# Kernel tuning notes

Measured on AMD Instinct MI355X. Metric: run time of the kernel, lower is better.

## Reference

```python
import jax, jax.numpy as jnp
import numpy as np

C = 256
C8 = C // 8
B, D, H, W = 2, 16, 64, 64


def setup_inputs() -> dict:
    key = jax.random.key(0)
    ks = jax.random.split(key, 8)
    s = 0.05
    return {
        "x1": jax.random.normal(ks[0], (B, C, D, H, W), dtype=jnp.float32),
        "x2": jax.random.normal(ks[1], (B, C, D, H, W), dtype=jnp.float32),
        "Wq": jax.random.normal(ks[2], (C8, C), dtype=jnp.float32) * s,
        "bq": jax.random.normal(ks[3], (C8,), dtype=jnp.float32) * s,
        "Wk": jax.random.normal(ks[4], (C8, C), dtype=jnp.float32) * s,
        "bk": jax.random.normal(ks[5], (C8,), dtype=jnp.float32) * s,
        "Wv": jax.random.normal(ks[6], (C, C), dtype=jnp.float32) * s,
        "bv": jax.random.normal(ks[7], (C,), dtype=jnp.float32) * s,
    }


def _conv1x1(x, Wt, b):
    # 1x1x1 Conv3d == channel-mixing linear: x [B,Cin,D,H,W], Wt [Cout,Cin]
    return jnp.einsum('bcdhw,oc->bodhw', x, Wt) + b[None, :, None, None, None]


def reference(x1, x2, Wq, bq, Wk, bk, Wv, bv):
    q = _conv1x1(x1, Wq, bq)   # [B,C8,D,H,W]
    k = _conv1x1(x2, Wk, bk)   # [B,C8,D,H,W]
    v = _conv1x1(x2, Wv, bv)   # [B,C, D,H,W]
    # Non-softmax bilinear attention over the W axis, batched over (b,d,h)
    attn = jnp.einsum('bcdhx,bcdhy->bdhxy', q, k)        # [B,D,H,W,W]
    out = jnp.einsum('bdhxy,bcdhy->bcdhx', attn, v)      # [B,C,D,H,W]
    return out
```

## Files before the change

kernel.cpp:

```cpp
#include <hip/hip_runtime.h>

#define NB   2
#define ND   16
#define NH   64
#define DHW  65536
#define HW   4096
#define CDHW 16777216

#define XT_LD 72
#define XL_LD 66
#define QK_LD 40
#define A_LD  72
#define VB_LD 72

#define OFF_XTH 0
#define OFF_XTL 9216
#define OFF_R2  18432
#define OFF_KH  18432
#define OFF_KL  23552
#define OFF_AH  0
#define OFF_AL  9216
#define OFF_QH  36864
#define OFF_QL  41984
#define SMEM_BYTES 47104

typedef __attribute__((ext_vector_type(4))) float f32x4;
typedef __attribute__((ext_vector_type(8))) short bf16x8;
typedef unsigned short ushort_t;

#define MFMA16(a, b, c) __builtin_amdgcn_mfma_f32_16x16x32_bf16((a), (b), (c), 0, 0, 0)

#define WS_WQH 0
#define WS_WQL 8192
#define WS_WKH 16384
#define WS_WKL 24576
#define WS_WVH 32768
#define WS_WVL 98304
#define WS_NEED_BYTES 327680

__device__ __forceinline__ void split_val(float f, short& h, short& l) {
  unsigned int u = __builtin_bit_cast(unsigned int, f);
  h = (short)(unsigned short)(u >> 16);
  float fh = __builtin_bit_cast(float, u & 0xffff0000u);
  float r = f - fh;
  l = (short)(unsigned short)(__builtin_bit_cast(unsigned int, r) >> 16);
}

__device__ __forceinline__ void load_split8(const float* __restrict__ p, bf16x8& h8, bf16x8& l8) {
  float4 a = *(const float4*)p;
  float4 b = *(const float4*)(p + 4);
  float f[8] = {a.x, a.y, a.z, a.w, b.x, b.y, b.z, b.w};
#pragma unroll
  for (int j = 0; j < 8; ++j) {
    short hh, ll;
    split_val(f[j], hh, ll);
    h8[j] = hh; l8[j] = ll;
  }
}

__global__ void prep_w(const float* __restrict__ Wq, const float* __restrict__ Wk,
                       const float* __restrict__ Wv, ushort_t* __restrict__ ws) {
  int idx = blockIdx.x * 256 + threadIdx.x;
  const float* src; int off; ushort_t *H, *L;
  if (idx < 8192)       { src = Wq; off = idx;         H = ws + WS_WQH; L = ws + WS_WQL; }
  else if (idx < 16384) { src = Wk; off = idx - 8192;  H = ws + WS_WKH; L = ws + WS_WKL; }
  else if (idx < 81920) { src = Wv; off = idx - 16384; H = ws + WS_WVH; L = ws + WS_WVL; }
  else return;
  short h, l;
  split_val(src[off], h, l);
  H[off] = (ushort_t)h;
  L[off] = (ushort_t)l;
}

template<bool PW>
__global__ __launch_bounds__(256, 3) void xattn(
    const float* __restrict__ x1, const float* __restrict__ x2,
    const float* __restrict__ Wq, const float* __restrict__ bq,
    const float* __restrict__ Wk, const float* __restrict__ bk,
    const float* __restrict__ Wv, const float* __restrict__ bv,
    const ushort_t* __restrict__ wsp, float* __restrict__ out)
{
  __shared__ char smem[SMEM_BYTES];
  ushort_t* Xth  = (ushort_t*)(smem + OFF_XTH);
  ushort_t* Xtl  = (ushort_t*)(smem + OFF_XTL);
  float*    Xlin = (float*)(smem + OFF_R2);
  ushort_t* Kh   = (ushort_t*)(smem + OFF_KH);
  ushort_t* Kl   = (ushort_t*)(smem + OFF_KL);
  ushort_t* Vb   = (ushort_t*)(smem + OFF_R2);
  ushort_t* Ah   = (ushort_t*)(smem + OFF_AH);
  ushort_t* Al   = (ushort_t*)(smem + OFF_AL);
  ushort_t* Qh   = (ushort_t*)(smem + OFF_QH);
  ushort_t* Ql   = (ushort_t*)(smem + OFF_QL);

  const int tid  = threadIdx.x;
  const int lane = tid & 63;
  const int wv   = tid >> 6;
  const int l15  = lane & 15;
  const int g    = lane >> 4;

  const int grp = blockIdx.x;
  const int b   = grp >> 10;
  const int rem = grp & 1023;
  const int d   = rem >> 6;
  const int h   = rem & 63;
  const size_t base = (size_t)b * CDHW + (size_t)d * HW + (size_t)h * 64;

  const ushort_t* WqH = wsp + WS_WQH;
  const ushort_t* WqL = wsp + WS_WQL;
  const ushort_t* WkH = wsp + WS_WKH;
  const ushort_t* WkL = wsp + WS_WKL;
  const ushort_t* WvH = wsp + WS_WVH;
  const ushort_t* WvL = wsp + WS_WVL;

  auto passA = [&](const float* __restrict__ src) {
#pragma unroll
    for (int i = 0; i < 4; ++i) {
      int ch = 16 * wv + (lane >> 4) + 4 * i;
      int c4 = (lane & 15) << 2;
      float4 v = *(const float4*)(src + (size_t)ch * DHW + c4);
      *(float4*)&Xlin[ch * XL_LD + c4] = v;
    }
  };
  auto passB = [&]() {
#pragma unroll
    for (int bb = 0; bb < 2; ++bb) {
      int c0 = 16 * wv + 8 * bb;
      bf16x8 h8, l8;
#pragma unroll
      for (int j = 0; j < 8; ++j) {
        float f = Xlin[(c0 + j) * XL_LD + lane];
        short hh, ll;
        split_val(f, hh, ll);
        h8[j] = hh; l8[j] = ll;
      }
      *(bf16x8*)&Xth[lane * XT_LD + c0] = h8;
      *(bf16x8*)&Xtl[lane * XT_LD + c0] = l8;
    }
  };

  {
    f32x4 qacc[2];
#pragma unroll
    for (int mt = 0; mt < 2; ++mt) {
      int r0 = mt * 16 + 4 * g;
      qacc[mt] = (f32x4){bq[r0], bq[r0 + 1], bq[r0 + 2], bq[r0 + 3]};
    }
    for (int t = 0; t < 4; ++t) {
      passA(x1 + base + (size_t)t * 64 * DHW);
      __syncthreads();
      passB();
      __syncthreads();
#pragma unroll
      for (int ks = 0; ks < 2; ++ks) {
        const int ko = ks * 32 + 8 * g;
        const int kg = t * 64 + ko;
        bf16x8 bh = *(const bf16x8*)&Xth[(16 * wv + l15) * XT_LD + ko];
        bf16x8 bl = *(const bf16x8*)&Xtl[(16 * wv + l15) * XT_LD + ko];
#pragma unroll
        for (int mt = 0; mt < 2; ++mt) {
          bf16x8 wh, wl;
          if constexpr (PW) {
            wh = *(const bf16x8*)&WqH[(size_t)(mt * 16 + l15) * 256 + kg];
            wl = *(const bf16x8*)&WqL[(size_t)(mt * 16 + l15) * 256 + kg];
          } else {
            load_split8(Wq + (size_t)(mt * 16 + l15) * 256 + kg, wh, wl);
          }
          qacc[mt] = MFMA16(wh, bh, qacc[mt]);
          qacc[mt] = MFMA16(wh, bl, qacc[mt]);
          qacc[mt] = MFMA16(wl, bh, qacc[mt]);
        }
      }
      __syncthreads();
    }
    const int x = 16 * wv + l15;
#pragma unroll
    for (int mt = 0; mt < 2; ++mt)
#pragma unroll
      for (int r = 0; r < 4; ++r) {
        short hh, ll;
        split_val(qacc[mt][r], hh, ll);
        Qh[x * QK_LD + mt * 16 + 4 * g + r] = (ushort_t)hh;
        Ql[x * QK_LD + mt * 16 + 4 * g + r] = (ushort_t)ll;
      }
  }

  f32x4 vacc[4][4];
  {
    f32x4 kacc[2];
#pragma unroll
    for (int mt = 0; mt < 2; ++mt) {
      int r0 = mt * 16 + 4 * g;
      kacc[mt] = (f32x4){bk[r0], bk[r0 + 1], bk[r0 + 2], bk[r0 + 3]};
    }
#pragma unroll
    for (int mt = 0; mt < 4; ++mt) {
      int r0 = 64 * wv + mt * 16 + 4 * g;
      f32x4 bb = (f32x4){bv[r0], bv[r0 + 1], bv[r0 + 2], bv[r0 + 3]};
#pragma unroll
      for (int nt = 0; nt < 4; ++nt) vacc[mt][nt] = bb;
    }
    for (int t = 0; t < 4; ++t) {
      passA(x2 + base + (size_t)t * 64 * DHW);
      __syncthreads();
      passB();
      __syncthreads();
#pragma unroll
      for (int ks = 0; ks < 2; ++ks) {
        const int ko = ks * 32 + 8 * g;
        const int kg = t * 64 + ko;
        bf16x8 xh[4], xl[4];
#pragma unroll
        for (int nt = 0; nt < 4; ++nt) {
          xh[nt] = *(const bf16x8*)&Xth[(nt * 16 + l15) * XT_LD + ko];
          xl[nt] = *(const bf16x8*)&Xtl[(nt * 16 + l15) * XT_LD + ko];
        }
        {
          bf16x8 bh = *(const bf16x8*)&Xth[(16 * wv + l15) * XT_LD + ko];
          bf16x8 bl = *(const bf16x8*)&Xtl[(16 * wv + l15) * XT_LD + ko];
#pragma unroll
          for (int mt = 0; mt < 2; ++mt) {
            bf16x8 wh, wl;
            if constexpr (PW) {
              wh = *(const bf16x8*)&WkH[(size_t)(mt * 16 + l15) * 256 + kg];
              wl = *(const bf16x8*)&WkL[(size_t)(mt * 16 + l15) * 256 + kg];
            } else {
              load_split8(Wk + (size_t)(mt * 16 + l15) * 256 + kg, wh, wl);
            }
            kacc[mt] = MFMA16(wh, bh, kacc[mt]);
            kacc[mt] = MFMA16(wh, bl, kacc[mt]);
            kacc[mt] = MFMA16(wl, bh, kacc[mt]);
          }
        }
#pragma unroll
        for (int mt = 0; mt < 4; ++mt) {
          bf16x8 wh, wl;
          if constexpr (PW) {
            wh = *(const bf16x8*)&WvH[(size_t)(64 * wv + mt * 16 + l15) * 256 + kg];
            wl = *(const bf16x8*)&WvL[(size_t)(64 * wv + mt * 16 + l15) * 256 + kg];
          } else {
            load_split8(Wv + (size_t)(64 * wv + mt * 16 + l15) * 256 + kg, wh, wl);
          }
#pragma unroll
          for (int nt = 0; nt < 4; ++nt) {
            vacc[mt][nt] = MFMA16(wh, xh[nt], vacc[mt][nt]);
            vacc[mt][nt] = MFMA16(wh, xl[nt], vacc[mt][nt]);
            vacc[mt][nt] = MFMA16(wl, xh[nt], vacc[mt][nt]);
          }
        }
      }
      __syncthreads();
    }
    const int y = 16 * wv + l15;
#pragma unroll
    for (int mt = 0; mt < 2; ++mt)
#pragma unroll
      for (int r = 0; r < 4; ++r) {
        short hh, ll;
        split_val(kacc[mt][r], hh, ll);
        Kh[y * QK_LD + mt * 16 + 4 * g + r] = (ushort_t)hh;
        Kl[y * QK_LD + mt * 16 + 4 * g + r] = (ushort_t)ll;
      }
  }
  __syncthreads();

  {
    const int y = 16 * wv + l15;
    bf16x8 kh = *(const bf16x8*)&Kh[y * QK_LD + 8 * g];
    bf16x8 kl = *(const bf16x8*)&Kl[y * QK_LD + 8 * g];
    f32x4 acc[4];
#pragma unroll
    for (int mt = 0; mt < 4; ++mt) acc[mt] = (f32x4){0.f, 0.f, 0.f, 0.f};
#pragma unroll
    for (int mt = 0; mt < 4; ++mt) {
      bf16x8 qh = *(const bf16x8*)&Qh[(mt * 16 + l15) * QK_LD + 8 * g];
      bf16x8 ql = *(const bf16x8*)&Ql[(mt * 16 + l15) * QK_LD + 8 * g];
      acc[mt] = MFMA16(qh, kh, acc[mt]);
      acc[mt] = MFMA16(qh, kl, acc[mt]);
      acc[mt] = MFMA16(ql, kh, acc[mt]);
    }
#pragma unroll
    for (int mt = 0; mt < 4; ++mt)
#pragma unroll
      for (int r = 0; r < 4; ++r) {
        short hh, ll;
        split_val(acc[mt][r], hh, ll);
        Ah[(mt * 16 + 4 * g + r) * A_LD + y] = (ushort_t)hh;
        Al[(mt * 16 + 4 * g + r) * A_LD + y] = (ushort_t)ll;
      }
  }
  __syncthreads();

  {
    ushort_t* Vh = Vb + wv * 2304;
    ushort_t* Vl = Vh + 1152;
    const int cb = 64 * wv;
#pragma unroll
    for (int mt = 0; mt < 4; ++mt) {
#pragma unroll
      for (int nt = 0; nt < 4; ++nt)
#pragma unroll
        for (int r = 0; r < 4; ++r) {
          short hh, ll;
          split_val(vacc[mt][nt][r], hh, ll);
          Vh[(4 * g + r) * VB_LD + nt * 16 + l15] = (ushort_t)hh;
          Vl[(4 * g + r) * VB_LD + nt * 16 + l15] = (ushort_t)ll;
        }
      f32x4 oacc[4];
#pragma unroll
      for (int nt = 0; nt < 4; ++nt) oacc[nt] = (f32x4){0.f, 0.f, 0.f, 0.f};
#pragma unroll
      for (int ys = 0; ys < 2; ++ys) {
        const int yo = ys * 32 + 8 * g;
        bf16x8 vh8 = *(const bf16x8*)&Vh[l15 * VB_LD + yo];
        bf16x8 vl8 = *(const bf16x8*)&Vl[l15 * VB_LD + yo];
#pragma unroll
        for (int nt = 0; nt < 4; ++nt) {
          bf16x8 ah8 = *(const bf16x8*)&Ah[(nt * 16 + l15) * A_LD + yo];
          bf16x8 al8 = *(const bf16x8*)&Al[(nt * 16 + l15) * A_LD + yo];
          oacc[nt] = MFMA16(vh8, ah8, oacc[nt]);
          oacc[nt] = MFMA16(vh8, al8, oacc[nt]);
          oacc[nt] = MFMA16(vl8, ah8, oacc[nt]);
        }
      }
#pragma unroll
      for (int nt = 0; nt < 4; ++nt)
#pragma unroll
        for (int r = 0; r < 4; ++r)
          out[base + (size_t)(cb + mt * 16 + 4 * g + r) * DHW + nt * 16 + l15] = oacc[nt][r];
    }
  }
}

extern "C" void kernel_launch(void* const* d_in, const int* in_sizes, int n_in,
                              void* d_out, int out_size, void* d_ws, size_t ws_size,
                              hipStream_t stream)
{
  const float* x1 = (const float*)d_in[0];
  const float* x2 = (const float*)d_in[1];
  const float* Wq = (const float*)d_in[2];
  const float* bq = (const float*)d_in[3];
  const float* Wk = (const float*)d_in[4];
  const float* bk = (const float*)d_in[5];
  const float* Wv = (const float*)d_in[6];
  const float* bv = (const float*)d_in[7];
  float* out = (float*)d_out;

  const bool pw = (ws_size >= (size_t)WS_NEED_BYTES) && (d_ws != nullptr);
  if (pw) {
    ushort_t* ws = (ushort_t*)d_ws;
    hipLaunchKernelGGL(prep_w, dim3(320), dim3(256), 0, stream, Wq, Wk, Wv, ws);
    hipLaunchKernelGGL(xattn<true>, dim3(NB * ND * NH), dim3(256), 0, stream,
                       x1, x2, Wq, bq, Wk, bk, Wv, bv, ws, out);
  } else {
    hipLaunchKernelGGL(xattn<false>, dim3(NB * ND * NH), dim3(256), 0, stream,
                       x1, x2, Wq, bq, Wk, bk, Wv, bv, (const ushort_t*)nullptr, out);
  }
}
```

Baseline: 206.5 us.

## Prefetch input chunks into registers and use XOR-swizzled LDS transpose

Replaces the two-pass staging (global to an fp32 LDS buffer, then transpose and split into bf16 hi/lo tiles) with direct per-lane register loads that are converted in registers and written once into an XOR-swizzled LDS layout. The next chunk's global loads are issued right after the LDS write, so they overlap the MFMA work of the current chunk, and the trailing barrier per iteration is removed. This cuts LDS traffic and one barrier per chunk, and hides global latency. In exchange it costs 16 extra registers per thread for the prefetch buffer, which may put pressure on the 3-blocks-per-CU occupancy target.

```diff
diff --git a/kernel.cpp b/kernel.cpp
--- a/kernel.cpp
+++ b/kernel.cpp
@@ -7,19 +7,17 @@
 #define HW   4096
 #define CDHW 16777216
 
-#define XT_LD 72
-#define XL_LD 66
 #define QK_LD 40
 #define A_LD  72
 #define VB_LD 72
 
 #define OFF_XTH 0
-#define OFF_XTL 9216
+#define OFF_XTL 8192
+#define OFF_AH  0
+#define OFF_AL  9216
 #define OFF_R2  18432
 #define OFF_KH  18432
 #define OFF_KL  23552
-#define OFF_AH  0
-#define OFF_AL  9216
 #define OFF_QH  36864
 #define OFF_QL  41984
 #define SMEM_BYTES 47104
@@ -81,16 +79,15 @@
     const ushort_t* __restrict__ wsp, float* __restrict__ out)
 {
   __shared__ char smem[SMEM_BYTES];
-  ushort_t* Xth  = (ushort_t*)(smem + OFF_XTH);
-  ushort_t* Xtl  = (ushort_t*)(smem + OFF_XTL);
-  float*    Xlin = (float*)(smem + OFF_R2);
-  ushort_t* Kh   = (ushort_t*)(smem + OFF_KH);
-  ushort_t* Kl   = (ushort_t*)(smem + OFF_KL);
-  ushort_t* Vb   = (ushort_t*)(smem + OFF_R2);
-  ushort_t* Ah   = (ushort_t*)(smem + OFF_AH);
-  ushort_t* Al   = (ushort_t*)(smem + OFF_AL);
-  ushort_t* Qh   = (ushort_t*)(smem + OFF_QH);
-  ushort_t* Ql   = (ushort_t*)(smem + OFF_QL);
+  ushort_t* Xth = (ushort_t*)(smem + OFF_XTH);
+  ushort_t* Xtl = (ushort_t*)(smem + OFF_XTL);
+  ushort_t* Kh  = (ushort_t*)(smem + OFF_KH);
+  ushort_t* Kl  = (ushort_t*)(smem + OFF_KL);
+  ushort_t* Vb  = (ushort_t*)(smem + OFF_R2);
+  ushort_t* Ah  = (ushort_t*)(smem + OFF_AH);
+  ushort_t* Al  = (ushort_t*)(smem + OFF_AL);
+  ushort_t* Qh  = (ushort_t*)(smem + OFF_QH);
+  ushort_t* Ql  = (ushort_t*)(smem + OFF_QL);
 
   const int tid  = threadIdx.x;
   const int lane = tid & 63;
@@ -112,30 +109,41 @@
   const ushort_t* WvH = wsp + WS_WVH;
   const ushort_t* WvL = wsp + WS_WVL;
 
-  auto passA = [&](const float* __restrict__ src) {
-#pragma unroll
-    for (int i = 0; i < 4; ++i) {
-      int ch = 16 * wv + (lane >> 4) + 4 * i;
-      int c4 = (lane & 15) << 2;
-      float4 v = *(const float4*)(src + (size_t)ch * DHW + c4);
-      *(float4*)&Xlin[ch * XL_LD + c4] = v;
-    }
+  const float* x1p = x1 + base;
+  const float* x2p = x2 + base;
+
+  float pf[16];
+  auto issue_pf = [&](const float* __restrict__ src) {
+#pragma unroll
+    for (int j = 0; j < 16; ++j)
+      pf[j] = src[(size_t)(16 * wv + j) * DHW + lane];
   };
-  auto passB = [&]() {
-#pragma unroll
-    for (int bb = 0; bb < 2; ++bb) {
-      int c0 = 16 * wv + 8 * bb;
-      bf16x8 h8, l8;
-#pragma unroll
-      for (int j = 0; j < 8; ++j) {
-        float f = Xlin[(c0 + j) * XL_LD + lane];
-        short hh, ll;
-        split_val(f, hh, ll);
-        h8[j] = hh; l8[j] = ll;
-      }
-      *(bf16x8*)&Xth[lane * XT_LD + c0] = h8;
-      *(bf16x8*)&Xtl[lane * XT_LD + c0] = l8;
-    }
+  bf16x8 sh0, sl0, sh1, sl1;
+  auto cvt = [&]() {
+#pragma unroll
+    for (int j = 0; j < 8; ++j) {
+      short hh, ll;
+      split_val(pf[j], hh, ll);
+      sh0[j] = hh; sl0[j] = ll;
+    }
+#pragma unroll
+    for (int j = 0; j < 8; ++j) {
+      short hh, ll;
+      split_val(pf[8 + j], hh, ll);
+      sh1[j] = hh; sl1[j] = ll;
+    }
+  };
+  auto write_x = [&]() {
+    int c0 = 16 * wv;
+    int bo0 = lane * 128 + (((c0)     * 2) ^ ((lane & 7) << 4));
+    int bo1 = lane * 128 + (((c0 + 8) * 2) ^ ((lane & 7) << 4));
+    *(bf16x8*)((char*)Xth + bo0) = sh0;
+    *(bf16x8*)((char*)Xtl + bo0) = sl0;
+    *(bf16x8*)((char*)Xth + bo1) = sh1;
+    *(bf16x8*)((char*)Xtl + bo1) = sl1;
+  };
+  auto ldsx = [&](const ushort_t* B, int row, int ko) -> bf16x8 {
+    return *(const bf16x8*)((const char*)B + row * 128 + (((ko) * 2) ^ ((row & 7) << 4)));
   };
 
   {
@@ -145,17 +153,19 @@
       int r0 = mt * 16 + 4 * g;
       qacc[mt] = (f32x4){bq[r0], bq[r0 + 1], bq[r0 + 2], bq[r0 + 3]};
     }
+    issue_pf(x1p);
     for (int t = 0; t < 4; ++t) {
-      passA(x1 + base + (size_t)t * 64 * DHW);
+      cvt();
       __syncthreads();
-      passB();
+      write_x();
+      issue_pf(t < 3 ? x1p + (size_t)(t + 1) * 64 * DHW : x2p);
       __syncthreads();
 #pragma unroll
       for (int ks = 0; ks < 2; ++ks) {
         const int ko = ks * 32 + 8 * g;
         const int kg = t * 64 + ko;
-        bf16x8 bh = *(const bf16x8*)&Xth[(16 * wv + l15) * XT_LD + ko];
-        bf16x8 bl = *(const bf16x8*)&Xtl[(16 * wv + l15) * XT_LD + ko];
+        bf16x8 bh = ldsx(Xth, 16 * wv + l15, ko);
+        bf16x8 bl = ldsx(Xtl, 16 * wv + l15, ko);
 #pragma unroll
         for (int mt = 0; mt < 2; ++mt) {
           bf16x8 wh, wl;
@@ -170,7 +180,6 @@
           qacc[mt] = MFMA16(wl, bh, qacc[mt]);
         }
       }
-      __syncthreads();
     }
     const int x = 16 * wv + l15;
 #pragma unroll
@@ -200,9 +209,10 @@
       for (int nt = 0; nt < 4; ++nt) vacc[mt][nt] = bb;
     }
     for (int t = 0; t < 4; ++t) {
-      passA(x2 + base + (size_t)t * 64 * DHW);
+      cvt();
       __syncthreads();
-      passB();
+      write_x();
+      if (t < 3) issue_pf(x2p + (size_t)(t + 1) * 64 * DHW);
       __syncthreads();
 #pragma unroll
       for (int ks = 0; ks < 2; ++ks) {
@@ -211,12 +221,12 @@
         bf16x8 xh[4], xl[4];
 #pragma unroll
         for (int nt = 0; nt < 4; ++nt) {
-          xh[nt] = *(const bf16x8*)&Xth[(nt * 16 + l15) * XT_LD + ko];
-          xl[nt] = *(const bf16x8*)&Xtl[(nt * 16 + l15) * XT_LD + ko];
+          xh[nt] = ldsx(Xth, nt * 16 + l15, ko);
+          xl[nt] = ldsx(Xtl, nt * 16 + l15, ko);
         }
         {
-          bf16x8 bh = *(const bf16x8*)&Xth[(16 * wv + l15) * XT_LD + ko];
-          bf16x8 bl = *(const bf16x8*)&Xtl[(16 * wv + l15) * XT_LD + ko];
+          bf16x8 bh = ldsx(Xth, 16 * wv + l15, ko);
+          bf16x8 bl = ldsx(Xtl, 16 * wv + l15, ko);
 #pragma unroll
           for (int mt = 0; mt < 2; ++mt) {
             bf16x8 wh, wl;
@@ -248,7 +258,6 @@
           }
         }
       }
-      __syncthreads();
     }
     const int y = 16 * wv + l15;
 #pragma unroll
```

New measurement: 260.4 us. 26.1% more time.

## Prefetch next x tile into registers, swizzle LDS layouts, raise occupancy to 4

Applied to the files above, without the earlier changes.

Global loads for the next 64-channel slice of x are issued into registers before the MFMA work on the current slice, then written to LDS afterwards, so load latency overlaps compute and one barrier per iteration is dropped. Padded LDS strides are replaced by an XOR-swizzled 128-byte row layout, which shrinks shared memory from about 46KB to 40KB. Launch bounds move from 3 to 4 blocks per CU, and s_setprio is raised around the MFMA bursts. The costs are more register pressure from the prefetch buffers and vacc under a tighter register budget, so spills are possible.

```diff
diff --git a/kernel.cpp b/kernel.cpp
--- a/kernel.cpp
+++ b/kernel.cpp
@@ -7,22 +7,16 @@
 #define HW   4096
 #define CDHW 16777216
 
-#define XT_LD 72
-#define XL_LD 66
-#define QK_LD 40
-#define A_LD  72
-#define VB_LD 72
-
 #define OFF_XTH 0
-#define OFF_XTL 9216
-#define OFF_R2  18432
-#define OFF_KH  18432
-#define OFF_KL  23552
+#define OFF_XTL 8192
 #define OFF_AH  0
-#define OFF_AL  9216
-#define OFF_QH  36864
-#define OFF_QL  41984
-#define SMEM_BYTES 47104
+#define OFF_AL  8192
+#define OFF_R2  16384
+#define OFF_KH  16384
+#define OFF_KL  20480
+#define OFF_QH  32768
+#define OFF_QL  36864
+#define SMEM_BYTES 40960
 
 typedef __attribute__((ext_vector_type(4))) float f32x4;
 typedef __attribute__((ext_vector_type(8))) short bf16x8;
@@ -56,6 +50,10 @@
     split_val(f[j], hh, ll);
     h8[j] = hh; l8[j] = ll;
   }
+}
+
+__device__ __forceinline__ int swzb(int row, int colb) {
+  return row * 128 + (((colb) & ~15) ^ ((row & 7) << 4)) + ((colb) & 15);
 }
 
 __global__ void prep_w(const float* __restrict__ Wq, const float* __restrict__ Wk,
@@ -73,7 +71,7 @@
 }
 
 template<bool PW>
-__global__ __launch_bounds__(256, 3) void xattn(
+__global__ __launch_bounds__(256, 4) void xattn(
     const float* __restrict__ x1, const float* __restrict__ x2,
     const float* __restrict__ Wq, const float* __restrict__ bq,
     const float* __restrict__ Wk, const float* __restrict__ bk,
@@ -81,14 +79,13 @@
     const ushort_t* __restrict__ wsp, float* __restrict__ out)
 {
   __shared__ char smem[SMEM_BYTES];
-  ushort_t* Xth  = (ushort_t*)(smem + OFF_XTH);
-  ushort_t* Xtl  = (ushort_t*)(smem + OFF_XTL);
+  char*     XthB = smem + OFF_XTH;
+  char*     XtlB = smem + OFF_XTL;
   float*    Xlin = (float*)(smem + OFF_R2);
   ushort_t* Kh   = (ushort_t*)(smem + OFF_KH);
   ushort_t* Kl   = (ushort_t*)(smem + OFF_KL);
-  ushort_t* Vb   = (ushort_t*)(smem + OFF_R2);
-  ushort_t* Ah   = (ushort_t*)(smem + OFF_AH);
-  ushort_t* Al   = (ushort_t*)(smem + OFF_AL);
+  char*     AhB  = smem + OFF_AH;
+  char*     AlB  = smem + OFF_AL;
   ushort_t* Qh   = (ushort_t*)(smem + OFF_QH);
   ushort_t* Ql   = (ushort_t*)(smem + OFF_QL);
 
@@ -112,13 +109,22 @@
   const ushort_t* WvH = wsp + WS_WVH;
   const ushort_t* WvL = wsp + WS_WVL;
 
-  auto passA = [&](const float* __restrict__ src) {
+  const float* x1p = x1 + base;
+  const float* x2p = x2 + base;
+
+  float4 pf[4];
+  auto issue_pf = [&](const float* __restrict__ src) {
 #pragma unroll
     for (int i = 0; i < 4; ++i) {
-      int ch = 16 * wv + (lane >> 4) + 4 * i;
-      int c4 = (lane & 15) << 2;
-      float4 v = *(const float4*)(src + (size_t)ch * DHW + c4);
-      *(float4*)&Xlin[ch * XL_LD + c4] = v;
+      int ch = 16 * wv + g + 4 * i;
+      pf[i] = *(const float4*)(src + (size_t)ch * DHW + 4 * l15);
+    }
+  };
+  auto write_xlin = [&]() {
+#pragma unroll
+    for (int i = 0; i < 4; ++i) {
+      int ch = 16 * wv + g + 4 * i;
+      *(float4*)&Xlin[ch * 64 + 4 * l15] = pf[i];
     }
   };
   auto passB = [&]() {
@@ -128,14 +134,17 @@
       bf16x8 h8, l8;
 #pragma unroll
       for (int j = 0; j < 8; ++j) {
-        float f = Xlin[(c0 + j) * XL_LD + lane];
+        float f = Xlin[(c0 + j) * 64 + lane];
         short hh, ll;
         split_val(f, hh, ll);
         h8[j] = hh; l8[j] = ll;
       }
-      *(bf16x8*)&Xth[lane * XT_LD + c0] = h8;
-      *(bf16x8*)&Xtl[lane * XT_LD + c0] = l8;
-    }
+      *(bf16x8*)(XthB + swzb(lane, c0 * 2)) = h8;
+      *(bf16x8*)(XtlB + swzb(lane, c0 * 2)) = l8;
+    }
+  };
+  auto ldsx = [&](const char* B, int row, int ko) -> bf16x8 {
+    return *(const bf16x8*)(B + swzb(row, ko * 2));
   };
 
   {
@@ -145,17 +154,19 @@
       int r0 = mt * 16 + 4 * g;
       qacc[mt] = (f32x4){bq[r0], bq[r0 + 1], bq[r0 + 2], bq[r0 + 3]};
     }
+    issue_pf(x1p);
+    write_xlin();
+    __syncthreads();
     for (int t = 0; t < 4; ++t) {
-      passA(x1 + base + (size_t)t * 64 * DHW);
-      __syncthreads();
       passB();
       __syncthreads();
+      issue_pf(t < 3 ? x1p + (size_t)(t + 1) * 64 * DHW : x2p);
 #pragma unroll
       for (int ks = 0; ks < 2; ++ks) {
         const int ko = ks * 32 + 8 * g;
         const int kg = t * 64 + ko;
-        bf16x8 bh = *(const bf16x8*)&Xth[(16 * wv + l15) * XT_LD + ko];
-        bf16x8 bl = *(const bf16x8*)&Xtl[(16 * wv + l15) * XT_LD + ko];
+        bf16x8 bh = ldsx(XthB, 16 * wv + l15, ko);
+        bf16x8 bl = ldsx(XtlB, 16 * wv + l15, ko);
 #pragma unroll
         for (int mt = 0; mt < 2; ++mt) {
           bf16x8 wh, wl;
@@ -170,6 +181,7 @@
           qacc[mt] = MFMA16(wl, bh, qacc[mt]);
         }
       }
+      write_xlin();
       __syncthreads();
     }
     const int x = 16 * wv + l15;
@@ -179,8 +191,8 @@
       for (int r = 0; r < 4; ++r) {
         short hh, ll;
         split_val(qacc[mt][r], hh, ll);
-        Qh[x * QK_LD + mt * 16 + 4 * g + r] = (ushort_t)hh;
-        Ql[x * QK_LD + mt * 16 + 4 * g + r] = (ushort_t)ll;
+        Qh[x * 32 + mt * 16 + 4 * g + r] = (ushort_t)hh;
+        Ql[x * 32 + mt * 16 + 4 * g + r] = (ushort_t)ll;
       }
   }
 
@@ -200,10 +212,9 @@
       for (int nt = 0; nt < 4; ++nt) vacc[mt][nt] = bb;
     }
     for (int t = 0; t < 4; ++t) {
-      passA(x2 + base + (size_t)t * 64 * DHW);
-      __syncthreads();
       passB();
       __syncthreads();
+      if (t < 3) issue_pf(x2p + (size_t)(t + 1) * 64 * DHW);
 #pragma unroll
       for (int ks = 0; ks < 2; ++ks) {
         const int ko = ks * 32 + 8 * g;
@@ -211,12 +222,12 @@
         bf16x8 xh[4], xl[4];
 #pragma unroll
         for (int nt = 0; nt < 4; ++nt) {
-          xh[nt] = *(const bf16x8*)&Xth[(nt * 16 + l15) * XT_LD + ko];
-          xl[nt] = *(const bf16x8*)&Xtl[(nt * 16 + l15) * XT_LD + ko];
+          xh[nt] = ldsx(XthB, nt * 16 + l15, ko);
+          xl[nt] = ldsx(XtlB, nt * 16 + l15, ko);
         }
         {
-          bf16x8 bh = *(const bf16x8*)&Xth[(16 * wv + l15) * XT_LD + ko];
-          bf16x8 bl = *(const bf16x8*)&Xtl[(16 * wv + l15) * XT_LD + ko];
+          bf16x8 bh = ldsx(XthB, 16 * wv + l15, ko);
+          bf16x8 bl = ldsx(XtlB, 16 * wv + l15, ko);
 #pragma unroll
           for (int mt = 0; mt < 2; ++mt) {
             bf16x8 wh, wl;
@@ -231,6 +242,7 @@
             kacc[mt] = MFMA16(wl, bh, kacc[mt]);
           }
         }
+        __builtin_amdgcn_s_setprio(1);
 #pragma unroll
         for (int mt = 0; mt < 4; ++mt) {
           bf16x8 wh, wl;
@@ -247,33 +259,37 @@
             vacc[mt][nt] = MFMA16(wl, xh[nt], vacc[mt][nt]);
           }
         }
+        __builtin_amdgcn_s_setprio(0);
+      }
+      if (t < 3) {
+        write_xlin();
+      } else {
+        const int y = 16 * wv + l15;
+#pragma unroll
+        for (int mt = 0; mt < 2; ++mt)
+#pragma unroll
+          for (int r = 0; r < 4; ++r) {
+            short hh, ll;
+            split_val(kacc[mt][r], hh, ll);
+            Kh[y * 32 + mt * 16 + 4 * g + r] = (ushort_t)hh;
+            Kl[y * 32 + mt * 16 + 4 * g + r] = (ushort_t)ll;
+          }
       }
       __syncthreads();
     }
-    const int y = 16 * wv + l15;
-#pragma unroll
-    for (int mt = 0; mt < 2; ++mt)
-#pragma unroll
-      for (int r = 0; r < 4; ++r) {
-        short hh, ll;
-        split_val(kacc[mt][r], hh, ll);
-        Kh[y * QK_LD + mt * 16 + 4 * g + r] = (ushort_t)hh;
-        Kl[y * QK_LD + mt * 16 + 4 * g + r] = (ushort_t)ll;
-      }
-  }
-  __syncthreads();
+  }
 
   {
     const int y = 16 * wv + l15;
-    bf16x8 kh = *(const bf16x8*)&Kh[y * QK_LD + 8 * g];
-    bf16x8 kl = *(const bf16x8*)&Kl[y * QK_LD + 8 * g];
+    bf16x8 kh = *(const bf16x8*)&Kh[y * 32 + 8 * g];
+    bf16x8 kl = *(const bf16x8*)&Kl[y * 32 + 8 * g];
     f32x4 acc[4];
 #pragma unroll
     for (int mt = 0; mt < 4; ++mt) acc[mt] = (f32x4){0.f, 0.f, 0.f, 0.f};
 #pragma unroll
     for (int mt = 0; mt < 4; ++mt) {
-      bf16x8 qh = *(const bf16x8*)&Qh[(mt * 16 + l15) * QK_LD + 8 * g];
-      bf16x8 ql = *(const bf16x8*)&Ql[(mt * 16 + l15) * QK_LD + 8 * g];
+      bf16x8 qh = *(const bf16x8*)&Qh[(mt * 16 + l15) * 32 + 8 * g];
+      bf16x8 ql = *(const bf16x8*)&Ql[(mt * 16 + l15) * 32 + 8 * g];
       acc[mt] = MFMA16(qh, kh, acc[mt]);
       acc[mt] = MFMA16(qh, kl, acc[mt]);
       acc[mt] = MFMA16(ql, kh, acc[mt]);
@@ -284,15 +300,16 @@
       for (int r = 0; r < 4; ++r) {
         short hh, ll;
         split_val(acc[mt][r], hh, ll);
-        Ah[(mt * 16 + 4 * g + r) * A_LD + y] = (ushort_t)hh;
-        Al[(mt * 16 + 4 * g + r) * A_LD + y] = (ushort_t)ll;
+        int xr = mt * 16 + 4 * g + r;
+        *(ushort_t*)(AhB + swzb(xr, y * 2)) = (ushort_t)hh;
+        *(ushort_t*)(AlB + swzb(xr, y * 2)) = (ushort_t)ll;
       }
   }
   __syncthreads();
 
   {
-    ushort_t* Vh = Vb + wv * 2304;
-    ushort_t* Vl = Vh + 1152;
+    char* VhB = smem + OFF_R2 + wv * 4096;
+    char* VlB = VhB + 2048;
     const int cb = 64 * wv;
 #pragma unroll
     for (int mt = 0; mt < 4; ++mt) {
@@ -302,26 +319,29 @@
         for (int r = 0; r < 4; ++r) {
           short hh, ll;
           split_val(vacc[mt][nt][r], hh, ll);
-          Vh[(4 * g + r) * VB_LD + nt * 16 + l15] = (ushort_t)hh;
-          Vl[(4 * g + r) * VB_LD + nt * 16 + l15] = (ushort_t)ll;
+          int colb = (nt * 16 + l15) * 2;
+          *(ushort_t*)(VhB + swzb(4 * g + r, colb)) = (ushort_t)hh;
+          *(ushort_t*)(VlB + swzb(4 * g + r, colb)) = (ushort_t)ll;
         }
       f32x4 oacc[4];
 #pragma unroll
       for (int nt = 0; nt < 4; ++nt) oacc[nt] = (f32x4){0.f, 0.f, 0.f, 0.f};
+      __builtin_amdgcn_s_setprio(1);
 #pragma unroll
       for (int ys = 0; ys < 2; ++ys) {
         const int yo = ys * 32 + 8 * g;
-        bf16x8 vh8 = *(const bf16x8*)&Vh[l15 * VB_LD + yo];
-        bf16x8 vl8 = *(const bf16x8*)&Vl[l15 * VB_LD + yo];
+        bf16x8 vh8 = *(const bf16x8*)(VhB + swzb(l15, yo * 2));
+        bf16x8 vl8 = *(const bf16x8*)(VlB + swzb(l15, yo * 2));
 #pragma unroll
         for (int nt = 0; nt < 4; ++nt) {
-          bf16x8 ah8 = *(const bf16x8*)&Ah[(nt * 16 + l15) * A_LD + yo];
-          bf16x8 al8 = *(const bf16x8*)&Al[(nt * 16 + l15) * A_LD + yo];
+          bf16x8 ah8 = *(const bf16x8*)(AhB + swzb(nt * 16 + l15, yo * 2));
+          bf16x8 al8 = *(const bf16x8*)(AlB + swzb(nt * 16 + l15, yo * 2));
           oacc[nt] = MFMA16(vh8, ah8, oacc[nt]);
           oacc[nt] = MFMA16(vh8, al8, oacc[nt]);
           oacc[nt] = MFMA16(vl8, ah8, oacc[nt]);
         }
       }
+      __builtin_amdgcn_s_setprio(0);
 #pragma unroll
       for (int nt = 0; nt < 4; ++nt)
 #pragma unroll
```

Result: slower. 319.6 us (+54.7%).

## Split fused attention into Q/K projection kernel and V-projection/attention kernel

Applied to the files above, without the earlier changes.

Adds a qk_kernel that computes Q and K per (b,d,h) strip with async global-to-LDS triple-buffered loads and writes split bf16 hi/lo Q^T/K^T to workspace. A second kernel, xattn_v, splits the 256 output channels across two blocks, reads Q/K from workspace to form the attention matrix, and computes the V projection and output using swizzled LDS, register prefetch and setprio. This doubles the grid and removes serial Q/K work from the heavy kernel, at the cost of an extra workspace round-trip, recomputing attention twice per group, and reading x2 twice. The two-kernel path only runs when the workspace is large enough (about 34 MB); otherwise the old fused kernel is used.

```diff
diff --git a/kernel.cpp b/kernel.cpp
--- a/kernel.cpp
+++ b/kernel.cpp
@@ -7,23 +7,6 @@
 #define HW   4096
 #define CDHW 16777216
 
-#define XT_LD 72
-#define XL_LD 66
-#define QK_LD 40
-#define A_LD  72
-#define VB_LD 72
-
-#define OFF_XTH 0
-#define OFF_XTL 9216
-#define OFF_R2  18432
-#define OFF_KH  18432
-#define OFF_KL  23552
-#define OFF_AH  0
-#define OFF_AL  9216
-#define OFF_QH  36864
-#define OFF_QL  41984
-#define SMEM_BYTES 47104
-
 typedef __attribute__((ext_vector_type(4))) float f32x4;
 typedef __attribute__((ext_vector_type(8))) short bf16x8;
 typedef unsigned short ushort_t;
@@ -36,7 +19,13 @@
 #define WS_WKL 24576
 #define WS_WVH 32768
 #define WS_WVL 98304
-#define WS_NEED_BYTES 327680
+#define WS_WEIGHT_USHORTS 163840
+#define WS_QTH (WS_WEIGHT_USHORTS)
+#define WS_QTL (WS_QTH + 4194304)
+#define WS_KTH (WS_QTH + 8388608)
+#define WS_KTL (WS_QTH + 12582912)
+#define WS_FULL_BYTES ((size_t)(WS_WEIGHT_USHORTS + 16777216) * 2)
+#define WS_W_BYTES ((size_t)WS_WEIGHT_USHORTS * 2)
 
 __device__ __forceinline__ void split_val(float f, short& h, short& l) {
   unsigned int u = __builtin_bit_cast(unsigned int, f);
@@ -57,6 +46,14 @@
     h8[j] = hh; l8[j] = ll;
   }
 }
+
+__device__ __forceinline__ int swzb(int row, int colb) {
+  return row * 128 + (((colb) & ~15) ^ ((row & 7) << 4)) + ((colb) & 15);
+}
+
+#define GLOAD16(gp, lp) \
+  __builtin_amdgcn_global_load_lds((const __attribute__((address_space(1))) void*)(const void*)(gp), \
+                                   (__attribute__((address_space(3))) void*)(void*)(lp), 16, 0, 0)
 
 __global__ void prep_w(const float* __restrict__ Wq, const float* __restrict__ Wk,
                        const float* __restrict__ Wv, ushort_t* __restrict__ ws) {
@@ -72,8 +69,334 @@
   L[off] = (ushort_t)l;
 }
 
+__global__ __launch_bounds__(256, 3) void qk_kernel(
+    const float* __restrict__ x1, const float* __restrict__ x2,
+    const float* __restrict__ bq, const float* __restrict__ bk,
+    ushort_t* __restrict__ ws)
+{
+  __shared__ char asmem[49152];
+  const int tid  = threadIdx.x;
+  const int lane = tid & 63;
+  const int wv   = tid >> 6;
+  const int l15  = lane & 15;
+  const int g    = lane >> 4;
+
+  const int task  = blockIdx.x * 4 + wv;
+  const int grp   = task >> 2;
+  const int strip = task & 3;
+  const int b   = grp >> 10;
+  const int rem = grp & 1023;
+  const int d   = rem >> 6;
+  const int h   = rem & 63;
+  const size_t base = (size_t)b * CDHW + (size_t)d * HW + (size_t)h * 64 + strip * 16;
+
+  const float* x1p = x1 + base;
+  const float* x2p = x2 + base;
+  char* bufs = asmem + wv * 12288;
+
+  const ushort_t* WqH = ws + WS_WQH;
+  const ushort_t* WqL = ws + WS_WQL;
+  const ushort_t* WkH = ws + WS_WKH;
+  const ushort_t* WkL = ws + WS_WKL;
+
+  const size_t loff = (size_t)(lane >> 2) * DHW + (size_t)(lane & 3) * 4;
+
+  f32x4 qacc[2], kacc[2];
+#pragma unroll
+  for (int mt = 0; mt < 2; ++mt) {
+    int r0 = mt * 16 + 4 * g;
+    qacc[mt] = (f32x4){bq[r0], bq[r0 + 1], bq[r0 + 2], bq[r0 + 3]};
+    kacc[mt] = (f32x4){bk[r0], bk[r0 + 1], bk[r0 + 2], bk[r0 + 3]};
+  }
+
+  auto issue = [&](int i) {
+    const int t = i >> 1, s = i & 1;
+    const float* src = (s == 0 ? x1p : x2p) + (size_t)t * 64 * DHW;
+    char* lb = bufs + (i % 3) * 4096;
+#pragma unroll
+    for (int k = 0; k < 4; ++k) {
+      const float* gp = src + (size_t)(16 * k) * DHW + loff;
+      GLOAD16(gp, lb + k * 1024);
+    }
+  };
+
+  issue(0); issue(1); issue(2);
+#pragma unroll
+  for (int i = 0; i < 8; ++i) {
+    if (i < 6)       asm volatile("s_waitcnt vmcnt(8)" ::: "memory");
+    else if (i == 6) asm volatile("s_waitcnt vmcnt(4)" ::: "memory");
+    else             asm volatile("s_waitcnt vmcnt(0)" ::: "memory");
+
+    const int t = i >> 1;
+    const float* bufF = (const float*)(bufs + (i % 3) * 4096);
+    bf16x8 bh[2], bl[2];
+#pragma unroll
+    for (int ks = 0; ks < 2; ++ks) {
+#pragma unroll
+      for (int j = 0; j < 8; ++j) {
+        float f = bufF[(32 * ks + 8 * g + j) * 16 + l15];
+        short hh, ll;
+        split_val(f, hh, ll);
+        bh[ks][j] = hh; bl[ks][j] = ll;
+      }
+    }
+    asm volatile("s_waitcnt lgkmcnt(0)" ::: "memory");
+    if (i + 3 < 8) issue(i + 3);
+
+    const ushort_t* Wh = (i & 1) ? WkH : WqH;
+    const ushort_t* Wl = (i & 1) ? WkL : WqL;
+    f32x4* acc = (i & 1) ? kacc : qacc;
+#pragma unroll
+    for (int ks = 0; ks < 2; ++ks) {
+      const int kg = t * 64 + ks * 32 + 8 * g;
+#pragma unroll
+      for (int mt = 0; mt < 2; ++mt) {
+        bf16x8 wh = *(const bf16x8*)&Wh[(size_t)(mt * 16 + l15) * 256 + kg];
+        bf16x8 wl = *(const bf16x8*)&Wl[(size_t)(mt * 16 + l15) * 256 + kg];
+        acc[mt] = MFMA16(wh, bh[ks], acc[mt]);
+        acc[mt] = MFMA16(wh, bl[ks], acc[mt]);
+        acc[mt] = MFMA16(wl, bh[ks], acc[mt]);
+      }
+    }
+  }
+
+  ushort_t* QTh = ws + WS_QTH + grp * 2048;
+  ushort_t* QTl = ws + WS_QTL + grp * 2048;
+  ushort_t* KTh = ws + WS_KTH + grp * 2048;
+  ushort_t* KTl = ws + WS_KTL + grp * 2048;
+  const int xrow = strip * 16 + l15;
+#pragma unroll
+  for (int mt = 0; mt < 2; ++mt) {
+    unsigned int h01 = 0, h23 = 0, l01 = 0, l23 = 0;
+    short hh, ll;
+    split_val(qacc[mt][0], hh, ll); h01 = (ushort_t)hh;            l01 = (ushort_t)ll;
+    split_val(qacc[mt][1], hh, ll); h01 |= ((unsigned)(ushort_t)hh) << 16; l01 |= ((unsigned)(ushort_t)ll) << 16;
+    split_val(qacc[mt][2], hh, ll); h23 = (ushort_t)hh;            l23 = (ushort_t)ll;
+    split_val(qacc[mt][3], hh, ll); h23 |= ((unsigned)(ushort_t)hh) << 16; l23 |= ((unsigned)(ushort_t)ll) << 16;
+    int off = xrow * 32 + mt * 16 + 4 * g;
+    uint2 vh; vh.x = h01; vh.y = h23;
+    uint2 vl; vl.x = l01; vl.y = l23;
+    *(uint2*)&QTh[off] = vh;
+    *(uint2*)&QTl[off] = vl;
+    split_val(kacc[mt][0], hh, ll); h01 = (ushort_t)hh;            l01 = (ushort_t)ll;
+    split_val(kacc[mt][1], hh, ll); h01 |= ((unsigned)(ushort_t)hh) << 16; l01 |= ((unsigned)(ushort_t)ll) << 16;
+    split_val(kacc[mt][2], hh, ll); h23 = (ushort_t)hh;            l23 = (ushort_t)ll;
+    split_val(kacc[mt][3], hh, ll); h23 |= ((unsigned)(ushort_t)hh) << 16; l23 |= ((unsigned)(ushort_t)ll) << 16;
+    vh.x = h01; vh.y = h23;
+    vl.x = l01; vl.y = l23;
+    *(uint2*)&KTh[off] = vh;
+    *(uint2*)&KTl[off] = vl;
+  }
+}
+
+#define B_OFF_XTH 0
+#define B_OFF_XTL 8192
+#define B_OFF_AH  16384
+#define B_OFF_AL  24576
+#define B_OFF_XLIN 32768
+#define B_SMEM 49152
+
+__global__ __launch_bounds__(256, 3) void xattn_v(
+    const float* __restrict__ x2, const float* __restrict__ bv,
+    const ushort_t* __restrict__ wsp, float* __restrict__ out)
+{
+  __shared__ char smem[B_SMEM];
+  char*  XthB = smem + B_OFF_XTH;
+  char*  XtlB = smem + B_OFF_XTL;
+  char*  AhB  = smem + B_OFF_AH;
+  char*  AlB  = smem + B_OFF_AL;
+  float* Xlin = (float*)(smem + B_OFF_XLIN);
+
+  const int tid  = threadIdx.x;
+  const int lane = tid & 63;
+  const int wv   = tid >> 6;
+  const int l15  = lane & 15;
+  const int g    = lane >> 4;
+
+  const int bid   = blockIdx.x;
+  const int grp   = bid >> 1;
+  const int chalf = bid & 1;
+  const int cbase = chalf * 128;
+  const int b   = grp >> 10;
+  const int rem = grp & 1023;
+  const int d   = rem >> 6;
+  const int h   = rem & 63;
+  const size_t base = (size_t)b * CDHW + (size_t)d * HW + (size_t)h * 64;
+  const float* x2p = x2 + base;
+
+  const ushort_t* WvH = wsp + WS_WVH;
+  const ushort_t* WvL = wsp + WS_WVL;
+
+  float4 pf[4];
+  auto issue_pf = [&](const float* __restrict__ src) {
+#pragma unroll
+    for (int i = 0; i < 4; ++i) {
+      int ch = 16 * wv + g + 4 * i;
+      pf[i] = *(const float4*)(src + (size_t)ch * DHW + 4 * l15);
+    }
+  };
+  auto write_xlin = [&]() {
+#pragma unroll
+    for (int i = 0; i < 4; ++i) {
+      int ch = 16 * wv + g + 4 * i;
+      *(float4*)&Xlin[ch * 64 + 4 * l15] = pf[i];
+    }
+  };
+  auto passB = [&]() {
+#pragma unroll
+    for (int bb = 0; bb < 2; ++bb) {
+      int c0 = 16 * wv + 8 * bb;
+      bf16x8 h8, l8;
+#pragma unroll
+      for (int j = 0; j < 8; ++j) {
+        float f = Xlin[(c0 + j) * 64 + lane];
+        short hh, ll;
+        split_val(f, hh, ll);
+        h8[j] = hh; l8[j] = ll;
+      }
+      *(bf16x8*)(XthB + swzb(lane, c0 * 2)) = h8;
+      *(bf16x8*)(XtlB + swzb(lane, c0 * 2)) = l8;
+    }
+  };
+  auto ldsx = [&](const char* B, int row, int ko) -> bf16x8 {
+    return *(const bf16x8*)(B + swzb(row, ko * 2));
+  };
+
+  f32x4 vacc[2][4];
+#pragma unroll
+  for (int mt = 0; mt < 2; ++mt) {
+    int r0 = cbase + 32 * wv + mt * 16 + 4 * g;
+    f32x4 bb = (f32x4){bv[r0], bv[r0 + 1], bv[r0 + 2], bv[r0 + 3]};
+#pragma unroll
+    for (int nt = 0; nt < 4; ++nt) vacc[mt][nt] = bb;
+  }
+
+  issue_pf(x2p);
+  {
+    const ushort_t* QTh = wsp + WS_QTH + grp * 2048;
+    const ushort_t* QTl = wsp + WS_QTL + grp * 2048;
+    const ushort_t* KTh = wsp + WS_KTH + grp * 2048;
+    const ushort_t* KTl = wsp + WS_KTL + grp * 2048;
+    const int y = 16 * wv + l15;
+    bf16x8 kh = *(const bf16x8*)&KTh[y * 32 + 8 * g];
+    bf16x8 kl = *(const bf16x8*)&KTl[y * 32 + 8 * g];
+    f32x4 acc[4];
+#pragma unroll
+    for (int mt = 0; mt < 4; ++mt) acc[mt] = (f32x4){0.f, 0.f, 0.f, 0.f};
+#pragma unroll
+    for (int mt = 0; mt < 4; ++mt) {
+      bf16x8 qh = *(const bf16x8*)&QTh[(mt * 16 + l15) * 32 + 8 * g];
+      bf16x8 ql = *(const bf16x8*)&QTl[(mt * 16 + l15) * 32 + 8 * g];
+      acc[mt] = MFMA16(qh, kh, acc[mt]);
+      acc[mt] = MFMA16(qh, kl, acc[mt]);
+      acc[mt] = MFMA16(ql, kh, acc[mt]);
+    }
+#pragma unroll
+    for (int mt = 0; mt < 4; ++mt)
+#pragma unroll
+      for (int r = 0; r < 4; ++r) {
+        short hh, ll;
+        split_val(acc[mt][r], hh, ll);
+        int xr = mt * 16 + 4 * g + r;
+        *(ushort_t*)(AhB + swzb(xr, y * 2)) = (ushort_t)hh;
+        *(ushort_t*)(AlB + swzb(xr, y * 2)) = (ushort_t)ll;
+      }
+  }
+  write_xlin();
+  __syncthreads();
+
+  for (int t = 0; t < 4; ++t) {
+    passB();
+    __syncthreads();
+    if (t < 3) issue_pf(x2p + (size_t)(t + 1) * 64 * DHW);
+#pragma unroll
+    for (int ks = 0; ks < 2; ++ks) {
+      const int ko = ks * 32 + 8 * g;
+      const int kg = t * 64 + ko;
+      bf16x8 xh[4], xl[4];
+#pragma unroll
+      for (int nt = 0; nt < 4; ++nt) {
+        xh[nt] = ldsx(XthB, nt * 16 + l15, ko);
+        xl[nt] = ldsx(XtlB, nt * 16 + l15, ko);
+      }
+      __builtin_amdgcn_s_setprio(1);
+#pragma unroll
+      for (int mt = 0; mt < 2; ++mt) {
+        bf16x8 wh = *(const bf16x8*)&WvH[(size_t)(cbase + 32 * wv + mt * 16 + l15) * 256 + kg];
+        bf16x8 wl = *(const bf16x8*)&WvL[(size_t)(cbase + 32 * wv + mt * 16 + l15) * 256 + kg];
+#pragma unroll
+        for (int nt = 0; nt < 4; ++nt) {
+          vacc[mt][nt] = MFMA16(wh, xh[nt], vacc[mt][nt]);
+          vacc[mt][nt] = MFMA16(wh, xl[nt], vacc[mt][nt]);
+          vacc[mt][nt] = MFMA16(wl, xh[nt], vacc[mt][nt]);
+        }
+      }
+      __builtin_amdgcn_s_setprio(0);
+    }
+    if (t < 3) write_xlin();
+    __syncthreads();
+  }
+
+  {
+    char* VhB = smem + B_OFF_XTH + wv * 4096;
+    char* VlB = VhB + 2048;
+#pragma unroll
+    for (int mt = 0; mt < 2; ++mt) {
+#pragma unroll
+      for (int nt = 0; nt < 4; ++nt)
+#pragma unroll
+        for (int r = 0; r < 4; ++r) {
+          short hh, ll;
+          split_val(vacc[mt][nt][r], hh, ll);
+          int colb = (nt * 16 + l15) * 2;
+          *(ushort_t*)(VhB + swzb(4 * g + r, colb)) = (ushort_t)hh;
+          *(ushort_t*)(VlB + swzb(4 * g + r, colb)) = (ushort_t)ll;
+        }
+      f32x4 oacc[4];
+#pragma unroll
+      for (int nt = 0; nt < 4; ++nt) oacc[nt] = (f32x4){0.f, 0.f, 0.f, 0.f};
+      __builtin_amdgcn_s_setprio(1);
+#pragma unroll
+      for (int ys = 0; ys < 2; ++ys) {
+        const int yo = ys * 32 + 8 * g;
+        bf16x8 vh8 = *(const bf16x8*)(VhB + swzb(l15, yo * 2));
+        bf16x8 vl8 = *(const bf16x8*)(VlB + swzb(l15, yo * 2));
+#pragma unroll
+        for (int nt = 0; nt < 4; ++nt) {
+          bf16x8 ah8 = *(const bf16x8*)(AhB + swzb(nt * 16 + l15, yo * 2));
+          bf16x8 al8 = *(const bf16x8*)(AlB + swzb(nt * 16 + l15, yo * 2));
+          oacc[nt] = MFMA16(vh8, ah8, oacc[nt]);
+          oacc[nt] = MFMA16(vh8, al8, oacc[nt]);
+          oacc[nt] = MFMA16(vl8, ah8, oacc[nt]);
+        }
+      }
+      __builtin_amdgcn_s_setprio(0);
+#pragma unroll
+      for (int nt = 0; nt < 4; ++nt)
+#pragma unroll
+        for (int r = 0; r < 4; ++r)
+          out[base + (size_t)(cbase + 32 * wv + mt * 16 + 4 * g + r) * DHW + nt * 16 + l15] = oacc[nt][r];
+    }
+  }
+}
+
+#define XT_LD 72
+#define QK_LD 40
+#define A_LD  72
+#define VB_LD 72
+#define OFF_XTH 0
+#define OFF_XTL 9216
+#define OFF_R2  18432
+#define OFF_KH  18432
+#define OFF_KL  23552
+#define OFF_AH  0
+#define OFF_AL  9216
+#define OFF_QH  36864
+#define OFF_QL  41984
+#define SMEM_BYTES 47104
+
 template<bool PW>
-__global__ __launch_bounds__(256, 3) void xattn(
+__global__ __launch_bounds__(256, 3) void xattn_fused(
     const float* __restrict__ x1, const float* __restrict__ x2,
     const float* __restrict__ Wq, const float* __restrict__ bq,
     const float* __restrict__ Wk, const float* __restrict__ bk,
@@ -118,7 +441,7 @@
       int ch = 16 * wv + (lane >> 4) + 4 * i;
       int c4 = (lane & 15) << 2;
       float4 v = *(const float4*)(src + (size_t)ch * DHW + c4);
-      *(float4*)&Xlin[ch * XL_LD + c4] = v;
+      *(float4*)&Xlin[ch * 66 + c4] = v;
     }
   };
   auto passB = [&]() {
@@ -128,7 +451,7 @@
       bf16x8 h8, l8;
 #pragma unroll
       for (int j = 0; j < 8; ++j) {
-        float f = Xlin[(c0 + j) * XL_LD + lane];
+        float f = Xlin[(c0 + j) * 66 + lane];
         short hh, ll;
         split_val(f, hh, ll);
         h8[j] = hh; l8[j] = ll;
@@ -145,8 +468,9 @@
       int r0 = mt * 16 + 4 * g;
       qacc[mt] = (f32x4){bq[r0], bq[r0 + 1], bq[r0 + 2], bq[r0 + 3]};
     }
+    const float* x1p = x1 + base;
     for (int t = 0; t < 4; ++t) {
-      passA(x1 + base + (size_t)t * 64 * DHW);
+      passA(x1p + (size_t)t * 64 * DHW);
       __syncthreads();
       passB();
       __syncthreads();
@@ -199,8 +523,9 @@
 #pragma unroll
       for (int nt = 0; nt < 4; ++nt) vacc[mt][nt] = bb;
     }
+    const float* x2p = x2 + base;
     for (int t = 0; t < 4; ++t) {
-      passA(x2 + base + (size_t)t * 64 * DHW);
+      passA(x2p + (size_t)t * 64 * DHW);
       __syncthreads();
       passB();
       __syncthreads();
@@ -345,14 +670,18 @@
   const float* bv = (const float*)d_in[7];
   float* out = (float*)d_out;
 
-  const bool pw = (ws_size >= (size_t)WS_NEED_BYTES) && (d_ws != nullptr);
-  if (pw) {
+  if (d_ws && ws_size >= WS_FULL_BYTES) {
     ushort_t* ws = (ushort_t*)d_ws;
     hipLaunchKernelGGL(prep_w, dim3(320), dim3(256), 0, stream, Wq, Wk, Wv, ws);
-    hipLaunchKernelGGL(xattn<true>, dim3(NB * ND * NH), dim3(256), 0, stream,
+    hipLaunchKernelGGL(qk_kernel, dim3(2048), dim3(256), 0, stream, x1, x2, bq, bk, ws);
+    hipLaunchKernelGGL(xattn_v, dim3(4096), dim3(256), 0, stream, x2, bv, ws, out);
+  } else if (d_ws && ws_size >= WS_W_BYTES) {
+    ushort_t* ws = (ushort_t*)d_ws;
+    hipLaunchKernelGGL(prep_w, dim3(320), dim3(256), 0, stream, Wq, Wk, Wv, ws);
+    hipLaunchKernelGGL(xattn_fused<true>, dim3(2048), dim3(256), 0, stream,
                        x1, x2, Wq, bq, Wk, bk, Wv, bv, ws, out);
   } else {
-    hipLaunchKernelGGL(xattn<false>, dim3(NB * ND * NH), dim3(256), 0, stream,
+    hipLaunchKernelGGL(xattn_fused<false>, dim3(2048), dim3(256), 0, stream,
                        x1, x2, Wq, bq, Wk, bk, Wv, bv, (const ushort_t*)nullptr, out);
   }
 }
```

Measured after the change: 275.4 us. 33.3% more time.
